# Optimization experiments

Measured on AMD Instinct MI355X. Metric: run time of the kernel, lower is better.

Reference implementation:

```python
import jax, jax.numpy as jnp
import numpy as np

B, V, NQ, D, HEADS, FF, NL = 2, 8, 336, 256, 8, 1024, 6
H_IMG, W_IMG = 512, 512


def setup_inputs() -> dict:
    key = jax.random.key(0)
    ks = iter(jax.random.split(key, 48))
    def n(shape, s=0.02):
        return jax.random.normal(next(ks), shape, dtype=jnp.float32) * s
    inp = {}
    inp["tgt"] = jnp.zeros((B, NQ, D), jnp.float32)
    inp["query_pos"] = jax.random.normal(next(ks), (B, NQ, D), jnp.float32)
    inp["reference_points"] = jax.random.uniform(next(ks), (B, NQ, 3), dtype=jnp.float32)
    inp["feat0"] = jax.random.normal(next(ks), (B, V, D, 64, 64), jnp.float32)
    inp["feat1"] = jax.random.normal(next(ks), (B, V, D, 32, 32), jnp.float32)
    inp["feat2"] = jax.random.normal(next(ks), (B, V, D, 16, 16), jnp.float32)
    # cameras: near-identity rotations, translation pushed +2 in z so points project in front
    inp["camera_R"] = jnp.broadcast_to(jnp.eye(3, dtype=jnp.float32), (B, V, 3, 3)) + n((B, V, 3, 3), 0.1)
    T = n((B, V, 3), 0.1)
    inp["camera_T"] = T.at[..., 2].add(2.0)
    K = jnp.array([[500.0, 0.0, 256.0], [0.0, 500.0, 256.0], [0.0, 0.0, 1.0]], jnp.float32)
    inp["camera_K"] = jnp.broadcast_to(K, (B, V, 3, 3))
    # decoder params (stacked over NL layers)
    inp["Wqkv"] = n((NL, 3 * D, D)); inp["bqkv"] = jnp.zeros((NL, 3 * D), jnp.float32)
    inp["Wo"] = n((NL, D, D));       inp["bo"] = jnp.zeros((NL, D), jnp.float32)
    inp["ln1_g"] = jnp.ones((NL, D), jnp.float32); inp["ln1_b"] = jnp.zeros((NL, D), jnp.float32)
    inp["Wproj"] = n((NL, D, D));    inp["bproj"] = jnp.zeros((NL, D), jnp.float32)
    inp["pn_g"] = jnp.ones((NL, D), jnp.float32); inp["pn_b"] = jnp.zeros((NL, D), jnp.float32)
    inp["W1"] = n((NL, FF, D));      inp["b1"] = jnp.zeros((NL, FF), jnp.float32)
    inp["W2"] = n((NL, D, FF));      inp["b2"] = jnp.zeros((NL, D), jnp.float32)
    inp["ln2_g"] = jnp.ones((NL, D), jnp.float32); inp["ln2_b"] = jnp.zeros((NL, D), jnp.float32)
    inp["pose_W0"] = n((D, D)); inp["pose_b0"] = jnp.zeros((D,), jnp.float32)
    inp["pose_W1"] = n((D, D)); inp["pose_b1"] = jnp.zeros((D,), jnp.float32)
    inp["pose_W2"] = n((3, D)); inp["pose_b2"] = jnp.zeros((3,), jnp.float32)
    inp["cls_W"] = n((1, D));   inp["cls_b"] = jnp.zeros((1,), jnp.float32)
    return inp


def _layer_norm(x, g, b):
    m = x.mean(-1, keepdims=True)
    v = ((x - m) ** 2).mean(-1, keepdims=True)
    return (x - m) * jax.lax.rsqrt(v + 1e-5) * g + b


def _project(pts, R, T, K):
    # pts (B,NQ,3) -> cam coords per view: pts @ R^T + T
    p = jnp.einsum('bqc,bvdc->bvqd', pts, R) + T[:, :, None, :]  # (B,V,NQ,3)
    z = jnp.clip(p[..., 2], 0.1, None)
    fx = K[..., 0, 0][:, :, None]; fy = K[..., 1, 1][:, :, None]
    cx = K[..., 0, 2][:, :, None]; cy = K[..., 1, 2][:, :, None]
    u = p[..., 0] * fx / z + cx
    v = p[..., 1] * fy / z + cy
    un = 2.0 * u / (W_IMG - 1) - 1.0
    vn = 2.0 * v / (H_IMG - 1) - 1.0
    mask = (un > -1.0) & (un < 1.0) & (vn > -1.0) & (vn < 1.0) & (p[..., 2] > 0)
    return jnp.stack([un, vn], -1), mask  # (B,V,NQ,2), (B,V,NQ)


def _sample(feats, grid):
    # bilinear point sampling == F.grid_sample(align_corners=False, padding_mode='zeros')
    C, Hh, Ww = feats.shape[2], feats.shape[3], feats.shape[4]
    f = feats.reshape(B * V, C, Hh, Ww)
    g = grid.reshape(B * V, NQ, 2)
    x = (g[..., 0] + 1.0) * Ww * 0.5 - 0.5
    y = (g[..., 1] + 1.0) * Hh * 0.5 - 0.5
    x0f = jnp.floor(x); y0f = jnp.floor(y)
    ix0 = x0f.astype(jnp.int32); iy0 = y0f.astype(jnp.int32)
    ix1 = ix0 + 1; iy1 = iy0 + 1
    wx1 = (x - x0f)[:, None, :]; wx0 = 1.0 - wx1
    wy1 = (y - y0f)[:, None, :]; wy0 = 1.0 - wy1
    def gat(ix, iy):
        valid = ((ix >= 0) & (ix < Ww) & (iy >= 0) & (iy < Hh)).astype(f.dtype)[:, None, :]
        ixc = jnp.clip(ix, 0, Ww - 1); iyc = jnp.clip(iy, 0, Hh - 1)
        vals = jax.vmap(lambda ff, yy, xx: ff[:, yy, xx])(f, iyc, ixc)  # (BV,C,NQ)
        return vals * valid
    out = (gat(ix0, iy0) * wy0 * wx0 + gat(ix1, iy0) * wy0 * wx1 +
           gat(ix0, iy1) * wy1 * wx0 + gat(ix1, iy1) * wy1 * wx1)
    return out.reshape(B, V, C, NQ).transpose(0, 1, 3, 2)  # (B,V,NQ,C)


def _mha(xq, xv, Wqkv, bqkv, Wo, bo):
    hd = D // HEADS
    q = (xq @ Wqkv[:D].T + bqkv[:D]).reshape(B, NQ, HEADS, hd)
    k = (xq @ Wqkv[D:2 * D].T + bqkv[D:2 * D]).reshape(B, NQ, HEADS, hd)
    v = (xv @ Wqkv[2 * D:].T + bqkv[2 * D:]).reshape(B, NQ, HEADS, hd)
    att = jax.nn.softmax(jnp.einsum('bqhd,bkhd->bhqk', q, k) * (1.0 / np.sqrt(hd)), axis=-1)
    o = jnp.einsum('bhqk,bkhd->bqhd', att, v).reshape(B, NQ, D)
    return o @ Wo.T + bo


def reference(tgt, query_pos, reference_points, feat0, feat1, feat2, camera_R, camera_T, camera_K,
              Wqkv, bqkv, Wo, bo, ln1_g, ln1_b, Wproj, bproj, pn_g, pn_b,
              W1, b1, W2, b2, ln2_g, ln2_b,
              pose_W0, pose_b0, pose_W1, pose_b1, pose_W2, pose_b2, cls_W, cls_b):
    out = tgt
    ref = reference_points
    feats = (feat0, feat1, feat2)
    logits_all, poses_all = [], []
    for l in range(NL):
        # self-attention (dropout = eval identity)
        qk = out + query_pos
        out = _layer_norm(out + _mha(qk, out, Wqkv[l], bqkv[l], Wo[l], bo[l]), ln1_g[l], ln1_b[l])
        # projective attention: project 3D refs, grid-sample all levels, mask-fuse across views
        grid, mask = _project(ref, camera_R, camera_T, camera_K)
        ms = (_sample(feats[0], grid) + _sample(feats[1], grid) + _sample(feats[2], grid)) / 3.0
        vm = mask[..., None].astype(out.dtype)  # (B,V,NQ,1)
        fused = (ms * vm).sum(1) / jnp.clip(vm.sum(1), 1.0, None)  # (B,NQ,D)
        out = _layer_norm(out + fused @ Wproj[l].T + bproj[l], pn_g[l], pn_b[l])
        # FFN
        ffn = jax.nn.relu(out @ W1[l].T + b1[l]) @ W2[l].T + b2[l]
        out = _layer_norm(out + ffn, ln2_g[l], ln2_b[l])
        # iterative pose refinement + classification head
        h = jax.nn.relu(out @ pose_W0.T + pose_b0)
        h = jax.nn.relu(h @ pose_W1.T + pose_b1)
        ref = ref + h @ pose_W2.T + pose_b2
        logits_all.append(out @ cls_W.T + cls_b)
        poses_all.append(ref)
    # (NL,B,NQ,1) logits ++ (NL,B,NQ,3) poses -> (NL,B,NQ,4)
    return jnp.concatenate([jnp.stack(logits_all), jnp.stack(poses_all)], axis=-1)
```

## Files before the change

### kernel.cpp

```cpp
#include <hip/hip_runtime.h>
#include <math.h>

#define BB 2
#define VV 8
#define NQ 336
#define DD 256
#define HEADS 8
#define HD 32
#define FF 1024
#define NL 6
#define BQ (BB*NQ)
#define W_IMG 512
#define H_IMG 512
#define MROWS BQ

__device__ __forceinline__ void job_transpose3(float* tile, int b,
                                               const float* __restrict__ f0,
                                               const float* __restrict__ f1,
                                               const float* __restrict__ f2,
                                               float* __restrict__ o0,
                                               float* __restrict__ o1,
                                               float* __restrict__ o2) {
    const float* src; float* dst; int HW, ptiles;
    if (b < 4096)      { src = f0; dst = o0; HW = 4096; ptiles = 128; }
    else if (b < 5120) { b -= 4096; src = f1; dst = o1; HW = 1024; ptiles = 32; }
    else               { b -= 5120; src = f2; dst = o2; HW = 256;  ptiles = 8;  }
    int cg = b & 1;
    int pt = (b >> 1) % ptiles;
    int bv = (b >> 1) / ptiles;
    int d0 = cg * 128, p0 = pt * 32;
    int t = threadIdx.x;
    int chb = t >> 3, px4 = (t & 7) * 4;
    #pragma unroll
    for (int pass = 0; pass < 4; ++pass) {
        int ch = pass * 32 + chb;
        float4 v = *(const float4*)(src + ((size_t)(bv * DD + d0 + ch)) * HW + p0 + px4);
        tile[ch * 33 + px4 + 0] = v.x; tile[ch * 33 + px4 + 1] = v.y;
        tile[ch * 33 + px4 + 2] = v.z; tile[ch * 33 + px4 + 3] = v.w;
    }
    __syncthreads();
    int c4 = (t & 31) * 4, pxb = t >> 5;
    #pragma unroll
    for (int pass = 0; pass < 4; ++pass) {
        int px = pass * 8 + pxb;
        float4 o;
        o.x = tile[(c4 + 0) * 33 + px];
        o.y = tile[(c4 + 1) * 33 + px];
        o.z = tile[(c4 + 2) * 33 + px];
        o.w = tile[(c4 + 3) * 33 + px];
        *(float4*)(dst + ((size_t)bv * HW + p0 + px) * DD + d0 + c4) = o;
    }
}

__global__ __launch_bounds__(256) void init_k(const float* __restrict__ tgt,
                                              const float* __restrict__ qp,
                                              const float* __restrict__ refpts,
                                              float* __restrict__ x,
                                              float* __restrict__ xq,
                                              float* __restrict__ refb) {
    int i = blockIdx.x * 256 + threadIdx.x;
    float4 tv = ((const float4*)tgt)[i];
    float4 qv = ((const float4*)qp)[i];
    ((float4*)x)[i] = tv;
    ((float4*)xq)[i] = make_float4(tv.x + qv.x, tv.y + qv.y, tv.z + qv.z, tv.w + qv.w);
    if (i < BQ * 3) refb[i] = refpts[i];
}

__device__ __forceinline__ void job_qkv(float* sm, int bid,
                                        const float* __restrict__ Aq,
                                        const float* __restrict__ Ax,
                                        const float* __restrict__ W,
                                        const float* __restrict__ bias,
                                        float* __restrict__ Qp,
                                        float* __restrict__ Kp,
                                        float* __restrict__ Vp) {
    float* At = sm;
    float* Wt = sm + 1088;
    int t = threadIdx.x;
    int m0 = (bid % 21) * 32;
    int ncol = bid / 21;
    int n0 = ncol * 64;
    const float* A = (ncol < 8) ? Aq : Ax;
    int tx = t & 15, ty = t >> 4;
    int nc = n0 + tx * 4;
    float acc0[4], acc1[4];
    {
        float4 bv = *(const float4*)(bias + nc);
        acc0[0] = bv.x; acc0[1] = bv.y; acc0[2] = bv.z; acc0[3] = bv.w;
        acc1[0] = bv.x; acc1[1] = bv.y; acc1[2] = bv.z; acc1[3] = bv.w;
    }
    int am = t >> 3, ak4 = (t & 7) * 4;
    for (int kt = 0; kt < 8; ++kt) {
        int kk = kt * 32;
        __syncthreads();
        {
            float4 v = *(const float4*)(A + (size_t)(m0 + am) * DD + kk + ak4);
            At[(ak4 + 0) * 34 + am] = v.x; At[(ak4 + 1) * 34 + am] = v.y;
            At[(ak4 + 2) * 34 + am] = v.z; At[(ak4 + 3) * 34 + am] = v.w;
        }
        #pragma unroll
        for (int s = 0; s < 2; ++s) {
            int idx = t + s * 256;
            int wn = idx >> 3, wk4 = (idx & 7) * 4;
            float4 v = *(const float4*)(W + (size_t)(n0 + wn) * DD + kk + wk4);
            Wt[(wk4 + 0) * 68 + wn] = v.x; Wt[(wk4 + 1) * 68 + wn] = v.y;
            Wt[(wk4 + 2) * 68 + wn] = v.z; Wt[(wk4 + 3) * 68 + wn] = v.w;
        }
        __syncthreads();
        #pragma unroll
        for (int k = 0; k < 32; ++k) {
            float2 av = *(const float2*)&At[k * 34 + ty * 2];
            float4 wv = *(const float4*)&Wt[k * 68 + tx * 4];
            acc0[0] = fmaf(av.x, wv.x, acc0[0]); acc0[1] = fmaf(av.x, wv.y, acc0[1]);
            acc0[2] = fmaf(av.x, wv.z, acc0[2]); acc0[3] = fmaf(av.x, wv.w, acc0[3]);
            acc1[0] = fmaf(av.y, wv.x, acc1[0]); acc1[1] = fmaf(av.y, wv.y, acc1[1]);
            acc1[2] = fmaf(av.y, wv.z, acc1[2]); acc1[3] = fmaf(av.y, wv.w, acc1[3]);
        }
    }
    int mr = m0 + ty * 2;
    int kind = nc >> 8;
    float* base = kind == 0 ? Qp : (kind == 1 ? Kp : Vp);
    int h = (nc >> 5) & 7, d4 = nc & 31;
    #pragma unroll
    for (int i = 0; i < 2; ++i) {
        int m = mr + i;
        int b = m / NQ, q = m - b * NQ;
        float* p = base + ((size_t)((b << 3) + h) * NQ + q) * HD + d4;
        float* src = i == 0 ? acc0 : acc1;
        *(float4*)p = make_float4(src[0], src[1], src[2], src[3]);
    }
}

__device__ __forceinline__ void job_pose(float* sm, int job,
                                         const float* __restrict__ x,
                                         const float* __restrict__ W0, const float* __restrict__ b0,
                                         const float* __restrict__ W1p, const float* __restrict__ b1p,
                                         const float* __restrict__ W2p, const float* __restrict__ b2p,
                                         const float* __restrict__ cW, const float* __restrict__ cb,
                                         float* __restrict__ refb, float* __restrict__ outp) {
    float* sX  = sm;
    float* sH  = sm + 1024;
    float* red = sm + 2048;
    int r0 = job * 4;
    int tid = threadIdx.x;
    ((float4*)sX)[tid] = ((const float4*)(x + (size_t)r0 * DD))[tid];
    __syncthreads();
    {
        float a0 = b0[tid], a1 = a0, a2 = a0, a3 = a0;
        const float* wp = W0 + (size_t)tid * DD;
        for (int k = 0; k < DD; k += 4) {
            float4 w  = *(const float4*)(wp + k);
            float4 x0 = *(const float4*)(sX + 0 * DD + k);
            float4 x1 = *(const float4*)(sX + 1 * DD + k);
            float4 x2 = *(const float4*)(sX + 2 * DD + k);
            float4 x3 = *(const float4*)(sX + 3 * DD + k);
            a0 = fmaf(x0.x, w.x, a0); a0 = fmaf(x0.y, w.y, a0); a0 = fmaf(x0.z, w.z, a0); a0 = fmaf(x0.w, w.w, a0);
            a1 = fmaf(x1.x, w.x, a1); a1 = fmaf(x1.y, w.y, a1); a1 = fmaf(x1.z, w.z, a1); a1 = fmaf(x1.w, w.w, a1);
            a2 = fmaf(x2.x, w.x, a2); a2 = fmaf(x2.y, w.y, a2); a2 = fmaf(x2.z, w.z, a2); a2 = fmaf(x2.w, w.w, a2);
            a3 = fmaf(x3.x, w.x, a3); a3 = fmaf(x3.y, w.y, a3); a3 = fmaf(x3.z, w.z, a3); a3 = fmaf(x3.w, w.w, a3);
        }
        sH[0 * DD + tid] = fmaxf(a0, 0.f);
        sH[1 * DD + tid] = fmaxf(a1, 0.f);
        sH[2 * DD + tid] = fmaxf(a2, 0.f);
        sH[3 * DD + tid] = fmaxf(a3, 0.f);
    }
    __syncthreads();
    float h[4];
    {
        float a0 = b1p[tid], a1 = a0, a2 = a0, a3 = a0;
        const float* wp = W1p + (size_t)tid * DD;
        for (int k = 0; k < DD; k += 4) {
            float4 w  = *(const float4*)(wp + k);
            float4 x0 = *(const float4*)(sH + 0 * DD + k);
            float4 x1 = *(const float4*)(sH + 1 * DD + k);
            float4 x2 = *(const float4*)(sH + 2 * DD + k);
            float4 x3 = *(const float4*)(sH + 3 * DD + k);
            a0 = fmaf(x0.x, w.x, a0); a0 = fmaf(x0.y, w.y, a0); a0 = fmaf(x0.z, w.z, a0); a0 = fmaf(x0.w, w.w, a0);
            a1 = fmaf(x1.x, w.x, a1); a1 = fmaf(x1.y, w.y, a1); a1 = fmaf(x1.z, w.z, a1); a1 = fmaf(x1.w, w.w, a1);
            a2 = fmaf(x2.x, w.x, a2); a2 = fmaf(x2.y, w.y, a2); a2 = fmaf(x2.z, w.z, a2); a2 = fmaf(x2.w, w.w, a2);
            a3 = fmaf(x3.x, w.x, a3); a3 = fmaf(x3.y, w.y, a3); a3 = fmaf(x3.z, w.z, a3); a3 = fmaf(x3.w, w.w, a3);
        }
        h[0] = fmaxf(a0, 0.f); h[1] = fmaxf(a1, 0.f); h[2] = fmaxf(a2, 0.f); h[3] = fmaxf(a3, 0.f);
    }
    float w2a = W2p[tid], w2b = W2p[DD + tid], w2c = W2p[2 * DD + tid], cw = cW[tid];
    float v[4][4];
    #pragma unroll
    for (int r = 0; r < 4; ++r) {
        v[r][0] = h[r] * w2a;
        v[r][1] = h[r] * w2b;
        v[r][2] = h[r] * w2c;
        v[r][3] = sX[r * DD + tid] * cw;
    }
    #pragma unroll
    for (int o2 = 32; o2 > 0; o2 >>= 1) {
        #pragma unroll
        for (int r = 0; r < 4; ++r) {
            #pragma unroll
            for (int c = 0; c < 4; ++c) v[r][c] += __shfl_xor(v[r][c], o2);
        }
    }
    int wid = tid >> 6, lane = tid & 63;
    if (lane == 0) {
        #pragma unroll
        for (int r = 0; r < 4; ++r) {
            #pragma unroll
            for (int c = 0; c < 4; ++c) red[(r * 4 + c) * 4 + wid] = v[r][c];
        }
    }
    __syncthreads();
    if (tid < 4) {
        int r = tid;
        float d0 = red[(r * 4 + 0) * 4 + 0] + red[(r * 4 + 0) * 4 + 1] + red[(r * 4 + 0) * 4 + 2] + red[(r * 4 + 0) * 4 + 3] + b2p[0];
        float d1 = red[(r * 4 + 1) * 4 + 0] + red[(r * 4 + 1) * 4 + 1] + red[(r * 4 + 1) * 4 + 2] + red[(r * 4 + 1) * 4 + 3] + b2p[1];
        float d2 = red[(r * 4 + 2) * 4 + 0] + red[(r * 4 + 2) * 4 + 1] + red[(r * 4 + 2) * 4 + 2] + red[(r * 4 + 2) * 4 + 3] + b2p[2];
        float cl = red[(r * 4 + 3) * 4 + 0] + red[(r * 4 + 3) * 4 + 1] + red[(r * 4 + 3) * 4 + 2] + red[(r * 4 + 3) * 4 + 3] + cb[0];
        int row = r0 + r;
        float rx = refb[(size_t)row * 3 + 0] + d0;
        float ry = refb[(size_t)row * 3 + 1] + d1;
        float rz = refb[(size_t)row * 3 + 2] + d2;
        refb[(size_t)row * 3 + 0] = rx;
        refb[(size_t)row * 3 + 1] = ry;
        refb[(size_t)row * 3 + 2] = rz;
        outp[(size_t)row * 4 + 0] = cl;
        outp[(size_t)row * 4 + 1] = rx;
        outp[(size_t)row * 4 + 2] = ry;
        outp[(size_t)row * 4 + 3] = rz;
    }
}

__global__ __launch_bounds__(256) void qkv_pose(const float* __restrict__ xq,
                                                const float* __restrict__ x,
                                                const float* __restrict__ Wqkv,
                                                const float* __restrict__ bqkv,
                                                float* __restrict__ Qp,
                                                float* __restrict__ Kp,
                                                float* __restrict__ Vp,
                                                const float* __restrict__ pW0, const float* __restrict__ pb0,
                                                const float* __restrict__ pW1, const float* __restrict__ pb1,
                                                const float* __restrict__ pW2, const float* __restrict__ pb2,
                                                const float* __restrict__ cW, const float* __restrict__ cb,
                                                float* __restrict__ refb, float* __restrict__ outp) {
    __shared__ float sm[3264];
    if (blockIdx.x < 252)
        job_qkv(sm, blockIdx.x, xq, x, Wqkv, bqkv, Qp, Kp, Vp);
    else
        job_pose(sm, blockIdx.x - 252, x, pW0, pb0, pW1, pb1, pW2, pb2, cW, cb, refb, outp);
}

__global__ __launch_bounds__(256) void qkv_tr(const float* __restrict__ xq,
                                              const float* __restrict__ x,
                                              const float* __restrict__ Wqkv,
                                              const float* __restrict__ bqkv,
                                              float* __restrict__ Qp,
                                              float* __restrict__ Kp,
                                              float* __restrict__ Vp,
                                              const float* __restrict__ f0,
                                              const float* __restrict__ f1,
                                              const float* __restrict__ f2,
                                              float* __restrict__ o0,
                                              float* __restrict__ o1,
                                              float* __restrict__ o2) {
    __shared__ float sm[4224];
    if (blockIdx.x < 252)
        job_qkv(sm, blockIdx.x, xq, x, Wqkv, bqkv, Qp, Kp, Vp);
    else
        job_transpose3(sm, blockIdx.x - 252, f0, f1, f2, o0, o1, o2);
}

__global__ __launch_bounds__(256) void pose_only(const float* __restrict__ x,
                                                 const float* __restrict__ pW0, const float* __restrict__ pb0,
                                                 const float* __restrict__ pW1, const float* __restrict__ pb1,
                                                 const float* __restrict__ pW2, const float* __restrict__ pb2,
                                                 const float* __restrict__ cW, const float* __restrict__ cb,
                                                 float* __restrict__ refb, float* __restrict__ outp) {
    __shared__ float sm[2112];
    job_pose(sm, blockIdx.x, x, pW0, pb0, pW1, pb1, pW2, pb2, cW, cb, refb, outp);
}

__global__ __launch_bounds__(256) void attn_fused(const float* __restrict__ Qp,
                                                  const float* __restrict__ Kp,
                                                  const float* __restrict__ Vp,
                                                  float* __restrict__ O) {
    __shared__ float sm[15264];
    float* S   = sm;
    float* KT  = sm + 11008;
    float* U   = sm + 13184;
    float* inv = sm + 15232;
    int blk = blockIdx.x;
    int bh = blk & 15, qt = blk >> 4;
    int t = threadIdx.x;
    const float scale = 0.17677669529663687f;
    const float* Qb = Qp + (size_t)bh * NQ * HD;
    const float* Kb = Kp + (size_t)bh * NQ * HD;
    const float* Vb = Vp + (size_t)bh * NQ * HD;
    {
        int ql = t >> 3, d4 = (t & 7) * 4;
        int qg = qt * 32 + ql;
        float4 v = (qg < NQ) ? *(const float4*)(Qb + (size_t)qg * HD + d4)
                             : make_float4(0.f, 0.f, 0.f, 0.f);
        U[(d4 + 0) * 36 + ql] = v.x * scale;
        U[(d4 + 1) * 36 + ql] = v.y * scale;
        U[(d4 + 2) * 36 + ql] = v.z * scale;
        U[(d4 + 3) * 36 + ql] = v.w * scale;
    }
    int tx = t & 15, ty = t >> 4;
    for (int kt = 0; kt < 6; ++kt) {
        __syncthreads();
        #pragma unroll
        for (int s = 0; s < 2; ++s) {
            int idx = t + s * 256;
            int kl = idx >> 3, d4 = (idx & 7) * 4;
            int kg = kt * 64 + kl;
            float4 v = (kg < NQ) ? *(const float4*)(Kb + (size_t)kg * HD + d4)
                                 : make_float4(0.f, 0.f, 0.f, 0.f);
            KT[(d4 + 0) * 68 + kl] = v.x; KT[(d4 + 1) * 68 + kl] = v.y;
            KT[(d4 + 2) * 68 + kl] = v.z; KT[(d4 + 3) * 68 + kl] = v.w;
        }
        __syncthreads();
        float a0[4] = {0, 0, 0, 0}, a1[4] = {0, 0, 0, 0};
        #pragma unroll
        for (int k = 0; k < 32; ++k) {
            float2 qv = *(const float2*)&U[k * 36 + ty * 2];
            float4 kv = *(const float4*)&KT[k * 68 + tx * 4];
            a0[0] = fmaf(qv.x, kv.x, a0[0]); a0[1] = fmaf(qv.x, kv.y, a0[1]);
            a0[2] = fmaf(qv.x, kv.z, a0[2]); a0[3] = fmaf(qv.x, kv.w, a0[3]);
            a1[0] = fmaf(qv.y, kv.x, a1[0]); a1[1] = fmaf(qv.y, kv.y, a1[1]);
            a1[2] = fmaf(qv.y, kv.z, a1[2]); a1[3] = fmaf(qv.y, kv.w, a1[3]);
        }
        int col = kt * 64 + tx * 4;
        if (col < NQ) {
            *(float4*)&S[(ty * 2 + 0) * 344 + col] = make_float4(a0[0], a0[1], a0[2], a0[3]);
            *(float4*)&S[(ty * 2 + 1) * 344 + col] = make_float4(a1[0], a1[1], a1[2], a1[3]);
        }
    }
    __syncthreads();
    {
        int r = t >> 3, cg = t & 7;
        float* row = S + (size_t)r * 344;
        float m = -1e30f;
        for (int i = 0; i < 42; ++i) m = fmaxf(m, row[cg + 8 * i]);
        m = fmaxf(m, __shfl_xor(m, 1));
        m = fmaxf(m, __shfl_xor(m, 2));
        m = fmaxf(m, __shfl_xor(m, 4));
        float ssum = 0.f;
        for (int i = 0; i < 42; ++i) {
            float e = expf(row[cg + 8 * i] - m);
            row[cg + 8 * i] = e;
            ssum += e;
        }
        ssum += __shfl_xor(ssum, 1);
        ssum += __shfl_xor(ssum, 2);
        ssum += __shfl_xor(ssum, 4);
        if (cg == 0) inv[r] = 1.f / ssum;
    }
    int q = t >> 3, d0 = (t & 7) * 4;
    float acc[4] = {0, 0, 0, 0};
    for (int kt = 0; kt < 6; ++kt) {
        __syncthreads();
        #pragma unroll
        for (int s = 0; s < 2; ++s) {
            int idx = t + s * 256;
            int kl = idx >> 3, d4 = (idx & 7) * 4;
            int kg = kt * 64 + kl;
            float4 v = (kg < NQ) ? *(const float4*)(Vb + (size_t)kg * HD + d4)
                                 : make_float4(0.f, 0.f, 0.f, 0.f);
            *(float4*)&U[kl * 32 + d4] = v;
        }
        __syncthreads();
        int kmax = (kt == 5) ? 16 : 64;
        const float* Srow = S + (size_t)q * 344 + kt * 64;
        #pragma unroll 8
        for (int kk = 0; kk < kmax; ++kk) {
            float p = Srow[kk];
            float4 vv = *(const float4*)&U[kk * 32 + d0];
            acc[0] = fmaf(p, vv.x, acc[0]); acc[1] = fmaf(p, vv.y, acc[1]);
            acc[2] = fmaf(p, vv.z, acc[2]); acc[3] = fmaf(p, vv.w, acc[3]);
        }
    }
    float iv = inv[q];
    int qg = qt * 32 + q;
    int b = bh >> 3, h = bh & 7;
    if (qg < NQ)
        *(float4*)(O + ((size_t)(b * NQ + qg)) * DD + h * HD + d0) =
            make_float4(acc[0] * iv, acc[1] * iv, acc[2] * iv, acc[3] * iv);
}

__device__ __forceinline__ void job_gemm_ln(float* sm, int r0,
                                            const float* __restrict__ A,
                                            const float* __restrict__ Wt,
                                            const float* __restrict__ bias,
                                            const float* __restrict__ gam,
                                            const float* __restrict__ bet,
                                            float* __restrict__ x) {
    float* sA    = sm;
    float* redS  = sm + 1024;
    float* redS2 = sm + 1040;
    float* mu    = sm + 1056;
    float* ri    = sm + 1060;
    int j = threadIdx.x;
    ((float4*)sA)[j] = ((const float4*)(A + (size_t)r0 * DD))[j];
    __syncthreads();
    float acc0 = bias[j], acc1 = acc0, acc2 = acc0, acc3 = acc0;
    const float* wp = Wt + (size_t)j * DD;
    for (int k = 0; k < DD; k += 4) {
        float4 w  = *(const float4*)(wp + k);
        float4 a0 = *(const float4*)(sA + 0 * DD + k);
        float4 a1 = *(const float4*)(sA + 1 * DD + k);
        float4 a2 = *(const float4*)(sA + 2 * DD + k);
        float4 a3 = *(const float4*)(sA + 3 * DD + k);
        acc0 = fmaf(a0.x, w.x, acc0); acc0 = fmaf(a0.y, w.y, acc0); acc0 = fmaf(a0.z, w.z, acc0); acc0 = fmaf(a0.w, w.w, acc0);
        acc1 = fmaf(a1.x, w.x, acc1); acc1 = fmaf(a1.y, w.y, acc1); acc1 = fmaf(a1.z, w.z, acc1); acc1 = fmaf(a1.w, w.w, acc1);
        acc2 = fmaf(a2.x, w.x, acc2); acc2 = fmaf(a2.y, w.y, acc2); acc2 = fmaf(a2.z, w.z, acc2); acc2 = fmaf(a2.w, w.w, acc2);
        acc3 = fmaf(a3.x, w.x, acc3); acc3 = fmaf(a3.y, w.y, acc3); acc3 = fmaf(a3.z, w.z, acc3); acc3 = fmaf(a3.w, w.w, acc3);
    }
    float val[4];
    val[0] = x[(size_t)(r0 + 0) * DD + j] + acc0;
    val[1] = x[(size_t)(r0 + 1) * DD + j] + acc1;
    val[2] = x[(size_t)(r0 + 2) * DD + j] + acc2;
    val[3] = x[(size_t)(r0 + 3) * DD + j] + acc3;
    float s[4], s2[4];
    #pragma unroll
    for (int r = 0; r < 4; ++r) { s[r] = val[r]; s2[r] = val[r] * val[r]; }
    #pragma unroll
    for (int o2 = 32; o2 > 0; o2 >>= 1) {
        #pragma unroll
        for (int r = 0; r < 4; ++r) {
            s[r]  += __shfl_xor(s[r],  o2);
            s2[r] += __shfl_xor(s2[r], o2);
        }
    }
    int wid = j >> 6, lane = j & 63;
    if (lane == 0) {
        #pragma unroll
        for (int r = 0; r < 4; ++r) { redS[r * 4 + wid] = s[r]; redS2[r * 4 + wid] = s2[r]; }
    }
    __syncthreads();
    if (j < 4) {
        int r = j;
        float ts  = redS[r * 4 + 0]  + redS[r * 4 + 1]  + redS[r * 4 + 2]  + redS[r * 4 + 3];
        float ts2 = redS2[r * 4 + 0] + redS2[r * 4 + 1] + redS2[r * 4 + 2] + redS2[r * 4 + 3];
        float mean = ts * (1.f / DD);
        float var = ts2 * (1.f / DD) - mean * mean;
        mu[r] = mean;
        ri[r] = rsqrtf(var + 1e-5f);
    }
    __syncthreads();
    float g = gam[j], be = bet[j];
    #pragma unroll
    for (int r = 0; r < 4; ++r)
        x[(size_t)(r0 + r) * DD + j] = (val[r] - mu[r]) * ri[r] * g + be;
}

template <bool TRANSPOSED>
__device__ __forceinline__ void job_sample(float* sm, int row,
                                           const float* __restrict__ f0,
                                           const float* __restrict__ f1,
                                           const float* __restrict__ f2,
                                           const float* __restrict__ refb,
                                           const float* __restrict__ Rm,
                                           const float* __restrict__ Tm,
                                           const float* __restrict__ Km,
                                           float* __restrict__ fused) {
    float* sg    = sm;
    float* sPart = sm + 32;
    int t = threadIdx.x;
    int b = row / NQ;
    if (t < 8) {
        int bv = b * VV + t;
        const float* r = refb + (size_t)row * 3;
        const float* R = Rm + (size_t)bv * 9;
        const float* T = Tm + (size_t)bv * 3;
        const float* K = Km + (size_t)bv * 9;
        float p0 = R[0] * r[0] + R[1] * r[1] + R[2] * r[2] + T[0];
        float p1 = R[3] * r[0] + R[4] * r[1] + R[5] * r[2] + T[1];
        float p2 = R[6] * r[0] + R[7] * r[1] + R[8] * r[2] + T[2];
        float z = fmaxf(p2, 0.1f);
        float u  = p0 * K[0] / z + K[2];
        float vv = p1 * K[4] / z + K[5];
        float un = 2.f * u  / (float)(W_IMG - 1) - 1.f;
        float vn = 2.f * vv / (float)(H_IMG - 1) - 1.f;
        bool m = (un > -1.f) && (un < 1.f) && (vn > -1.f) && (vn < 1.f) && (p2 > 0.f);
        sg[t * 3 + 0] = un; sg[t * 3 + 1] = vn; sg[t * 3 + 2] = m ? 1.f : 0.f;
    }
    __syncthreads();
    int v = t >> 5, cg = t & 31;
    int ch0 = cg * 8;
    float acc[8] = {0, 0, 0, 0, 0, 0, 0, 0};
    float m = sg[v * 3 + 2];
    if (m != 0.f) {
        float un = sg[v * 3 + 0], vn = sg[v * 3 + 1];
        int bv = b * VV + v;
        const float* fl[3] = { f0, f1, f2 };
        const int Hs[3] = { 64, 32, 16 };
        #pragma unroll
        for (int lev = 0; lev < 3; ++lev) {
            int Hh = Hs[lev], Ww = Hs[lev];
            const float* f = fl[lev];
            float xx = (un + 1.f) * Ww * 0.5f - 0.5f;
            float yy = (vn + 1.f) * Hh * 0.5f - 0.5f;
            float x0f = floorf(xx), y0f = floorf(yy);
            int ix0 = (int)x0f, iy0 = (int)y0f;
            float wx1 = xx - x0f, wx0 = 1.f - wx1;
            float wy1 = yy - y0f, wy0 = 1.f - wy1;
            #pragma unroll
            for (int tap = 0; tap < 4; ++tap) {
                int ix = ix0 + (tap & 1);
                int iy = iy0 + (tap >> 1);
                float wgt = ((tap & 1) ? wx1 : wx0) * ((tap >> 1) ? wy1 : wy0);
                if (ix >= 0 && ix < Ww && iy >= 0 && iy < Hh) {
                    if (TRANSPOSED) {
                        const float* p = f + ((size_t)bv * Hh * Ww + (size_t)iy * Ww + ix) * DD + ch0;
                        float4 va = *(const float4*)p;
                        float4 vb = *(const float4*)(p + 4);
                        acc[0] = fmaf(wgt, va.x, acc[0]); acc[1] = fmaf(wgt, va.y, acc[1]);
                        acc[2] = fmaf(wgt, va.z, acc[2]); acc[3] = fmaf(wgt, va.w, acc[3]);
                        acc[4] = fmaf(wgt, vb.x, acc[4]); acc[5] = fmaf(wgt, vb.y, acc[5]);
                        acc[6] = fmaf(wgt, vb.z, acc[6]); acc[7] = fmaf(wgt, vb.w, acc[7]);
                    } else {
                        #pragma unroll
                        for (int c = 0; c < 8; ++c) {
                            float vv2 = f[(((size_t)bv * DD + ch0 + c) * Hh + iy) * Ww + ix];
                            acc[c] = fmaf(wgt, vv2, acc[c]);
                        }
                    }
                }
            }
        }
    }
    #pragma unroll
    for (int c = 0; c < 8; ++c) sPart[v * 258 + ch0 + c] = acc[c] * (1.f / 3.f);
    __syncthreads();
    float cnt = sg[2] + sg[5] + sg[8] + sg[11] + sg[14] + sg[17] + sg[20] + sg[23];
    float s = 0.f;
    #pragma unroll
    for (int v2 = 0; v2 < 8; ++v2) s += sPart[v2 * 258 + t];
    fused[(size_t)row * DD + t] = s / fmaxf(cnt, 1.f);
}

template <bool TRANSPOSED>
__global__ __launch_bounds__(256) void oproj_sample(const float* __restrict__ attn_o,
                                                    const float* __restrict__ Wo,
                                                    const float* __restrict__ bo,
                                                    const float* __restrict__ gam,
                                                    const float* __restrict__ bet,
                                                    float* __restrict__ x,
                                                    const float* __restrict__ f0,
                                                    const float* __restrict__ f1,
                                                    const float* __restrict__ f2,
                                                    const float* __restrict__ refb,
                                                    const float* __restrict__ Rm,
                                                    const float* __restrict__ Tm,
                                                    const float* __restrict__ Km,
                                                    float* __restrict__ fused) {
    __shared__ float sm[2112];
    if (blockIdx.x < 168)
        job_gemm_ln(sm, blockIdx.x * 4, attn_o, Wo, bo, gam, bet, x);
    else
        job_sample<TRANSPOSED>(sm, blockIdx.x - 168, f0, f1, f2, refb, Rm, Tm, Km, fused);
}

__global__ __launch_bounds__(256) void gemm4_res_ln(const float* __restrict__ A,
                                                    const float* __restrict__ Wt,
                                                    const float* __restrict__ bias,
                                                    const float* __restrict__ gam,
                                                    const float* __restrict__ bet,
                                                    float* __restrict__ x) {
    __shared__ float sm[1064];
    job_gemm_ln(sm, blockIdx.x * 4, A, Wt, bias, gam, bet, x);
}

template <int MODE>
__global__ __launch_bounds__(256) void gemm_tile(const float* __restrict__ A,
                                                 const float* __restrict__ W,
                                                 const float* __restrict__ bias,
                                                 float* __restrict__ C,
                                                 int Ktot, int Kper, int Nout) {
    __shared__ float At[32][34];
    __shared__ float Wt[32][68];
    int t = threadIdx.x;
    int m0 = blockIdx.x * 32;
    int n0 = blockIdx.y * 64;
    int kz = blockIdx.z;
    int kofs = kz * Kper;
    int tx = t & 15, ty = t >> 4;
    int nc = n0 + tx * 4;
    float acc0[4], acc1[4];
    {
        float4 bv = make_float4(0.f, 0.f, 0.f, 0.f);
        if (bias && kz == 0) bv = *(const float4*)(bias + nc);
        acc0[0] = bv.x; acc0[1] = bv.y; acc0[2] = bv.z; acc0[3] = bv.w;
        acc1[0] = bv.x; acc1[1] = bv.y; acc1[2] = bv.z; acc1[3] = bv.w;
    }
    int am = t >> 3, ak4 = (t & 7) * 4;
    int ktiles = Kper >> 5;
    for (int kt = 0; kt < ktiles; ++kt) {
        int kk = kofs + kt * 32;
        __syncthreads();
        {
            float4 v = *(const float4*)(A + (size_t)(m0 + am) * Ktot + kk + ak4);
            At[ak4 + 0][am] = v.x; At[ak4 + 1][am] = v.y;
            At[ak4 + 2][am] = v.z; At[ak4 + 3][am] = v.w;
        }
        #pragma unroll
        for (int s = 0; s < 2; ++s) {
            int idx = t + s * 256;
            int wn = idx >> 3, wk4 = (idx & 7) * 4;
            float4 v = *(const float4*)(W + (size_t)(n0 + wn) * Ktot + kk + wk4);
            Wt[wk4 + 0][wn] = v.x; Wt[wk4 + 1][wn] = v.y;
            Wt[wk4 + 2][wn] = v.z; Wt[wk4 + 3][wn] = v.w;
        }
        __syncthreads();
        #pragma unroll
        for (int k = 0; k < 32; ++k) {
            float2 av = *(const float2*)&At[k][ty * 2];
            float4 wv = *(const float4*)&Wt[k][tx * 4];
            acc0[0] = fmaf(av.x, wv.x, acc0[0]); acc0[1] = fmaf(av.x, wv.y, acc0[1]);
            acc0[2] = fmaf(av.x, wv.z, acc0[2]); acc0[3] = fmaf(av.x, wv.w, acc0[3]);
            acc1[0] = fmaf(av.y, wv.x, acc1[0]); acc1[1] = fmaf(av.y, wv.y, acc1[1]);
            acc1[2] = fmaf(av.y, wv.z, acc1[2]); acc1[3] = fmaf(av.y, wv.w, acc1[3]);
        }
    }
    if (MODE == 1) {
        #pragma unroll
        for (int j = 0; j < 4; ++j) { acc0[j] = fmaxf(acc0[j], 0.f); acc1[j] = fmaxf(acc1[j], 0.f); }
    }
    int mr = m0 + ty * 2;
    float* Cb = C + (size_t)kz * MROWS * Nout;
    *(float4*)(Cb + (size_t)mr * Nout + nc)       = make_float4(acc0[0], acc0[1], acc0[2], acc0[3]);
    *(float4*)(Cb + (size_t)(mr + 1) * Nout + nc) = make_float4(acc1[0], acc1[1], acc1[2], acc1[3]);
}

template <int NP>
__global__ __launch_bounds__(256) void ln_res(float* __restrict__ x,
                                              const float* __restrict__ C,
                                              const float* __restrict__ gam,
                                              const float* __restrict__ bet,
                                              const float* __restrict__ qp,
                                              float* __restrict__ xq) {
    __shared__ float redS[4][4], redS2[4][4];
    __shared__ float mu[4], ri[4];
    int r0 = blockIdx.x * 4;
    int j = threadIdx.x;
    float val[4];
    #pragma unroll
    for (int r = 0; r < 4; ++r) {
        float a = x[(size_t)(r0 + r) * DD + j];
        #pragma unroll
        for (int p = 0; p < NP; ++p) a += C[(size_t)p * MROWS * DD + (size_t)(r0 + r) * DD + j];
        val[r] = a;
    }
    float s[4], s2[4];
    #pragma unroll
    for (int r = 0; r < 4; ++r) { s[r] = val[r]; s2[r] = val[r] * val[r]; }
    #pragma unroll
    for (int o = 32; o > 0; o >>= 1) {
        #pragma unroll
        for (int r = 0; r < 4; ++r) {
            s[r]  += __shfl_xor(s[r],  o);
            s2[r] += __shfl_xor(s2[r], o);
        }
    }
    int wid = j >> 6, lane = j & 63;
    if (lane == 0) {
        #pragma unroll
        for (int r = 0; r < 4; ++r) { redS[r][wid] = s[r]; redS2[r][wid] = s2[r]; }
    }
    __syncthreads();
    if (j < 4) {
        int r = j;
        float ts  = redS[r][0]  + redS[r][1]  + redS[r][2]  + redS[r][3];
        float ts2 = redS2[r][0] + redS2[r][1] + redS2[r][2] + redS2[r][3];
        float mean = ts * (1.f / DD);
        float var = ts2 * (1.f / DD) - mean * mean;
        mu[r] = mean;
        ri[r] = rsqrtf(var + 1e-5f);
    }
    __syncthreads();
    float g = gam[j], be = bet[j];
    #pragma unroll
    for (int r = 0; r < 4; ++r) {
        float o = (val[r] - mu[r]) * ri[r] * g + be;
        x[(size_t)(r0 + r) * DD + j] = o;
        if (qp) xq[(size_t)(r0 + r) * DD + j] = o + qp[(size_t)(r0 + r) * DD + j];
    }
}

extern "C" void kernel_launch(void* const* d_in, const int* in_sizes, int n_in,
                              void* d_out, int out_size, void* d_ws, size_t ws_size,
                              hipStream_t stream) {
    const float* tgt       = (const float*)d_in[0];
    const float* query_pos = (const float*)d_in[1];
    const float* refpts    = (const float*)d_in[2];
    const float* feat0     = (const float*)d_in[3];
    const float* feat1     = (const float*)d_in[4];
    const float* feat2     = (const float*)d_in[5];
    const float* camR      = (const float*)d_in[6];
    const float* camT      = (const float*)d_in[7];
    const float* camK      = (const float*)d_in[8];
    const float* Wqkv      = (const float*)d_in[9];
    const float* bqkv      = (const float*)d_in[10];
    const float* Wo        = (const float*)d_in[11];
    const float* bo        = (const float*)d_in[12];
    const float* ln1_g     = (const float*)d_in[13];
    const float* ln1_b     = (const float*)d_in[14];
    const float* Wproj     = (const float*)d_in[15];
    const float* bproj     = (const float*)d_in[16];
    const float* pn_g      = (const float*)d_in[17];
    const float* pn_b      = (const float*)d_in[18];
    const float* W1        = (const float*)d_in[19];
    const float* b1        = (const float*)d_in[20];
    const float* W2        = (const float*)d_in[21];
    const float* b2        = (const float*)d_in[22];
    const float* ln2_g     = (const float*)d_in[23];
    const float* ln2_b     = (const float*)d_in[24];
    const float* pose_W0   = (const float*)d_in[25];
    const float* pose_b0   = (const float*)d_in[26];
    const float* pose_W1   = (const float*)d_in[27];
    const float* pose_b1   = (const float*)d_in[28];
    const float* pose_W2   = (const float*)d_in[29];
    const float* pose_b2   = (const float*)d_in[30];
    const float* cls_W     = (const float*)d_in[31];
    const float* cls_b     = (const float*)d_in[32];
    float* out = (float*)d_out;

    float* w = (float*)d_ws;
    size_t off = 0;
    auto alloc = [&](size_t n) { float* p = w + off; off += n; return p; };
    float* x      = alloc((size_t)BQ * DD);
    float* xq     = alloc((size_t)BQ * DD);
    float* Qp     = alloc((size_t)BB * HEADS * NQ * HD);
    float* Kp     = alloc((size_t)BB * HEADS * NQ * HD);
    float* Vp     = alloc((size_t)BB * HEADS * NQ * HD);
    float* attn_o = alloc((size_t)BQ * DD);
    float* fused  = alloc((size_t)BQ * DD);
    float* ffh    = alloc((size_t)BQ * FF);
    float* ctmp   = alloc((size_t)4 * BQ * DD);
    float* refb   = alloc((size_t)BQ * 3 + 64);
    size_t base_floats = off;
    size_t featT_floats = (size_t)BB * VV * DD * (64 * 64 + 32 * 32 + 16 * 16);
    bool useT = ws_size >= (base_floats + featT_floats) * sizeof(float);
    float *fT0 = nullptr, *fT1 = nullptr, *fT2 = nullptr;
    if (useT) {
        fT0 = alloc((size_t)BB * VV * 64 * 64 * DD);
        fT1 = alloc((size_t)BB * VV * 32 * 32 * DD);
        fT2 = alloc((size_t)BB * VV * 16 * 16 * DD);
    }

    init_k<<<168, 256, 0, stream>>>(tgt, query_pos, refpts, x, xq, refb);

    for (int l = 0; l < NL; ++l) {
        if (l == 0 && useT) {
            qkv_tr<<<252 + 5376, 256, 0, stream>>>(
                xq, x, Wqkv, bqkv, Qp, Kp, Vp,
                feat0, feat1, feat2, fT0, fT1, fT2);
        } else {
            qkv_pose<<<252 + (l > 0 ? 168 : 0), 256, 0, stream>>>(
                xq, x, Wqkv + (size_t)l * 3 * DD * DD, bqkv + (size_t)l * 3 * DD, Qp, Kp, Vp,
                pose_W0, pose_b0, pose_W1, pose_b1, pose_W2, pose_b2, cls_W, cls_b,
                refb, out + (size_t)(l - 1) * BQ * 4);
        }
        attn_fused<<<176, 256, 0, stream>>>(Qp, Kp, Vp, attn_o);
        if (useT)
            oproj_sample<true><<<840, 256, 0, stream>>>(
                attn_o, Wo + (size_t)l * DD * DD, bo + (size_t)l * DD,
                ln1_g + (size_t)l * DD, ln1_b + (size_t)l * DD, x,
                fT0, fT1, fT2, refb, camR, camT, camK, fused);
        else
            oproj_sample<false><<<840, 256, 0, stream>>>(
                attn_o, Wo + (size_t)l * DD * DD, bo + (size_t)l * DD,
                ln1_g + (size_t)l * DD, ln1_b + (size_t)l * DD, x,
                feat0, feat1, feat2, refb, camR, camT, camK, fused);
        gemm4_res_ln<<<BQ / 4, 256, 0, stream>>>(
            fused, Wproj + (size_t)l * DD * DD, bproj + (size_t)l * DD,
            pn_g + (size_t)l * DD, pn_b + (size_t)l * DD, x);
        gemm_tile<1><<<dim3(21, 16, 1), 256, 0, stream>>>(
            x, W1 + (size_t)l * FF * DD, b1 + (size_t)l * FF, ffh, DD, DD, FF);
        gemm_tile<0><<<dim3(21, 4, 4), 256, 0, stream>>>(
            ffh, W2 + (size_t)l * DD * FF, b2 + (size_t)l * DD, ctmp, FF, FF / 4, DD);
        ln_res<4><<<BQ / 4, 256, 0, stream>>>(
            x, ctmp, ln2_g + (size_t)l * DD, ln2_b + (size_t)l * DD, query_pos, xq);
    }
    pose_only<<<BQ / 4, 256, 0, stream>>>(
        x, pose_W0, pose_b0, pose_W1, pose_b1, pose_W2, pose_b2, cls_W, cls_b,
        refb, out + (size_t)(NL - 1) * BQ * 4);
}
```

Baseline: 842.7 us.

## Fuse attention with grid sampling and merge both output projections with layernorms

Attention now runs as 16-query-tile blocks inside the same launch as the multi-view grid-sampling blocks, which removes one launch per layer and lets the two independent stages overlap. The attention output projection with its layernorm and the fused-feature projection with its layernorm are merged into one kernel that handles two rows per block, keeping the intermediate row in shared memory. This works because sampling depends only on the reference points, not on the attention result. The cost is larger shared memory in the combined kernel, which may lower occupancy for the sampling blocks, and the two-rows-per-block GEMM rereads the weights more often.

```diff
diff --git a/kernel.cpp b/kernel.cpp
--- a/kernel.cpp
+++ b/kernel.cpp
@@ -277,33 +277,32 @@
     job_pose(sm, blockIdx.x, x, pW0, pb0, pW1, pb1, pW2, pb2, cW, cb, refb, outp);
 }
 
-__global__ __launch_bounds__(256) void attn_fused(const float* __restrict__ Qp,
-                                                  const float* __restrict__ Kp,
-                                                  const float* __restrict__ Vp,
-                                                  float* __restrict__ O) {
-    __shared__ float sm[15264];
+__device__ __forceinline__ void job_attn16(float* sm, int blk,
+                                           const float* __restrict__ Qp,
+                                           const float* __restrict__ Kp,
+                                           const float* __restrict__ Vp,
+                                           float* __restrict__ O) {
     float* S   = sm;
-    float* KT  = sm + 11008;
-    float* U   = sm + 13184;
-    float* inv = sm + 15232;
-    int blk = blockIdx.x;
+    float* KT  = sm + 5504;
+    float* U   = sm + 7680;
+    float* inv = sm + 9728;
     int bh = blk & 15, qt = blk >> 4;
     int t = threadIdx.x;
     const float scale = 0.17677669529663687f;
     const float* Qb = Qp + (size_t)bh * NQ * HD;
     const float* Kb = Kp + (size_t)bh * NQ * HD;
     const float* Vb = Vp + (size_t)bh * NQ * HD;
-    {
+    if (t < 128) {
         int ql = t >> 3, d4 = (t & 7) * 4;
-        int qg = qt * 32 + ql;
+        int qg = qt * 16 + ql;
         float4 v = (qg < NQ) ? *(const float4*)(Qb + (size_t)qg * HD + d4)
                              : make_float4(0.f, 0.f, 0.f, 0.f);
-        U[(d4 + 0) * 36 + ql] = v.x * scale;
-        U[(d4 + 1) * 36 + ql] = v.y * scale;
-        U[(d4 + 2) * 36 + ql] = v.z * scale;
-        U[(d4 + 3) * 36 + ql] = v.w * scale;
-    }
-    int tx = t & 15, ty = t >> 4;
+        U[(d4 + 0) * 20 + ql] = v.x * scale;
+        U[(d4 + 1) * 20 + ql] = v.y * scale;
+        U[(d4 + 2) * 20 + ql] = v.z * scale;
+        U[(d4 + 3) * 20 + ql] = v.w * scale;
+    }
+    int r = t >> 4, tx = t & 15;
     for (int kt = 0; kt < 6; ++kt) {
         __syncthreads();
         #pragma unroll
@@ -317,44 +316,41 @@
             KT[(d4 + 2) * 68 + kl] = v.z; KT[(d4 + 3) * 68 + kl] = v.w;
         }
         __syncthreads();
-        float a0[4] = {0, 0, 0, 0}, a1[4] = {0, 0, 0, 0};
+        float a0 = 0.f, a1 = 0.f, a2 = 0.f, a3 = 0.f;
         #pragma unroll
         for (int k = 0; k < 32; ++k) {
-            float2 qv = *(const float2*)&U[k * 36 + ty * 2];
+            float qv = U[k * 20 + r];
             float4 kv = *(const float4*)&KT[k * 68 + tx * 4];
-            a0[0] = fmaf(qv.x, kv.x, a0[0]); a0[1] = fmaf(qv.x, kv.y, a0[1]);
-            a0[2] = fmaf(qv.x, kv.z, a0[2]); a0[3] = fmaf(qv.x, kv.w, a0[3]);
-            a1[0] = fmaf(qv.y, kv.x, a1[0]); a1[1] = fmaf(qv.y, kv.y, a1[1]);
-            a1[2] = fmaf(qv.y, kv.z, a1[2]); a1[3] = fmaf(qv.y, kv.w, a1[3]);
+            a0 = fmaf(qv, kv.x, a0); a1 = fmaf(qv, kv.y, a1);
+            a2 = fmaf(qv, kv.z, a2); a3 = fmaf(qv, kv.w, a3);
         }
         int col = kt * 64 + tx * 4;
-        if (col < NQ) {
-            *(float4*)&S[(ty * 2 + 0) * 344 + col] = make_float4(a0[0], a0[1], a0[2], a0[3]);
-            *(float4*)&S[(ty * 2 + 1) * 344 + col] = make_float4(a1[0], a1[1], a1[2], a1[3]);
-        }
+        if (col < NQ)
+            *(float4*)&S[r * 344 + col] = make_float4(a0, a1, a2, a3);
     }
     __syncthreads();
     {
-        int r = t >> 3, cg = t & 7;
         float* row = S + (size_t)r * 344;
         float m = -1e30f;
-        for (int i = 0; i < 42; ++i) m = fmaxf(m, row[cg + 8 * i]);
+        for (int i = 0; i < 21; ++i) m = fmaxf(m, row[tx + 16 * i]);
         m = fmaxf(m, __shfl_xor(m, 1));
         m = fmaxf(m, __shfl_xor(m, 2));
         m = fmaxf(m, __shfl_xor(m, 4));
+        m = fmaxf(m, __shfl_xor(m, 8));
         float ssum = 0.f;
-        for (int i = 0; i < 42; ++i) {
-            float e = expf(row[cg + 8 * i] - m);
-            row[cg + 8 * i] = e;
+        for (int i = 0; i < 21; ++i) {
+            float e = expf(row[tx + 16 * i] - m);
+            row[tx + 16 * i] = e;
             ssum += e;
         }
         ssum += __shfl_xor(ssum, 1);
         ssum += __shfl_xor(ssum, 2);
         ssum += __shfl_xor(ssum, 4);
-        if (cg == 0) inv[r] = 1.f / ssum;
-    }
-    int q = t >> 3, d0 = (t & 7) * 4;
-    float acc[4] = {0, 0, 0, 0};
+        ssum += __shfl_xor(ssum, 8);
+        if (tx == 0) inv[r] = 1.f / ssum;
+    }
+    int d0 = tx * 2;
+    float acc0 = 0.f, acc1 = 0.f;
     for (int kt = 0; kt < 6; ++kt) {
         __syncthreads();
         #pragma unroll
@@ -368,87 +364,20 @@
         }
         __syncthreads();
         int kmax = (kt == 5) ? 16 : 64;
-        const float* Srow = S + (size_t)q * 344 + kt * 64;
+        const float* Srow = S + (size_t)r * 344 + kt * 64;
         #pragma unroll 8
         for (int kk = 0; kk < kmax; ++kk) {
             float p = Srow[kk];
-            float4 vv = *(const float4*)&U[kk * 32 + d0];
-            acc[0] = fmaf(p, vv.x, acc[0]); acc[1] = fmaf(p, vv.y, acc[1]);
-            acc[2] = fmaf(p, vv.z, acc[2]); acc[3] = fmaf(p, vv.w, acc[3]);
-        }
-    }
-    float iv = inv[q];
-    int qg = qt * 32 + q;
+            float2 vv = *(const float2*)&U[kk * 32 + d0];
+            acc0 = fmaf(p, vv.x, acc0); acc1 = fmaf(p, vv.y, acc1);
+        }
+    }
+    float iv = inv[r];
+    int qg = qt * 16 + r;
     int b = bh >> 3, h = bh & 7;
     if (qg < NQ)
-        *(float4*)(O + ((size_t)(b * NQ + qg)) * DD + h * HD + d0) =
-            make_float4(acc[0] * iv, acc[1] * iv, acc[2] * iv, acc[3] * iv);
-}
-
-__device__ __forceinline__ void job_gemm_ln(float* sm, int r0,
-                                            const float* __restrict__ A,
-                                            const float* __restrict__ Wt,
-                                            const float* __restrict__ bias,
-                                            const float* __restrict__ gam,
-                                            const float* __restrict__ bet,
-                                            float* __restrict__ x) {
-    float* sA    = sm;
-    float* redS  = sm + 1024;
-    float* redS2 = sm + 1040;
-    float* mu    = sm + 1056;
-    float* ri    = sm + 1060;
-    int j = threadIdx.x;
-    ((float4*)sA)[j] = ((const float4*)(A + (size_t)r0 * DD))[j];
-    __syncthreads();
-    float acc0 = bias[j], acc1 = acc0, acc2 = acc0, acc3 = acc0;
-    const float* wp = Wt + (size_t)j * DD;
-    for (int k = 0; k < DD; k += 4) {
-        float4 w  = *(const float4*)(wp + k);
-        float4 a0 = *(const float4*)(sA + 0 * DD + k);
-        float4 a1 = *(const float4*)(sA + 1 * DD + k);
-        float4 a2 = *(const float4*)(sA + 2 * DD + k);
-        float4 a3 = *(const float4*)(sA + 3 * DD + k);
-        acc0 = fmaf(a0.x, w.x, acc0); acc0 = fmaf(a0.y, w.y, acc0); acc0 = fmaf(a0.z, w.z, acc0); acc0 = fmaf(a0.w, w.w, acc0);
-        acc1 = fmaf(a1.x, w.x, acc1); acc1 = fmaf(a1.y, w.y, acc1); acc1 = fmaf(a1.z, w.z, acc1); acc1 = fmaf(a1.w, w.w, acc1);
-        acc2 = fmaf(a2.x, w.x, acc2); acc2 = fmaf(a2.y, w.y, acc2); acc2 = fmaf(a2.z, w.z, acc2); acc2 = fmaf(a2.w, w.w, acc2);
-        acc3 = fmaf(a3.x, w.x, acc3); acc3 = fmaf(a3.y, w.y, acc3); acc3 = fmaf(a3.z, w.z, acc3); acc3 = fmaf(a3.w, w.w, acc3);
-    }
-    float val[4];
-    val[0] = x[(size_t)(r0 + 0) * DD + j] + acc0;
-    val[1] = x[(size_t)(r0 + 1) * DD + j] + acc1;
-    val[2] = x[(size_t)(r0 + 2) * DD + j] + acc2;
-    val[3] = x[(size_t)(r0 + 3) * DD + j] + acc3;
-    float s[4], s2[4];
-    #pragma unroll
-    for (int r = 0; r < 4; ++r) { s[r] = val[r]; s2[r] = val[r] * val[r]; }
-    #pragma unroll
-    for (int o2 = 32; o2 > 0; o2 >>= 1) {
-        #pragma unroll
-        for (int r = 0; r < 4; ++r) {
-            s[r]  += __shfl_xor(s[r],  o2);
-            s2[r] += __shfl_xor(s2[r], o2);
-        }
-    }
-    int wid = j >> 6, lane = j & 63;
-    if (lane == 0) {
-        #pragma unroll
-        for (int r = 0; r < 4; ++r) { redS[r * 4 + wid] = s[r]; redS2[r * 4 + wid] = s2[r]; }
-    }
-    __syncthreads();
-    if (j < 4) {
-        int r = j;
-        float ts  = redS[r * 4 + 0]  + redS[r * 4 + 1]  + redS[r * 4 + 2]  + redS[r * 4 + 3];
-        float ts2 = redS2[r * 4 + 0] + redS2[r * 4 + 1] + redS2[r * 4 + 2] + redS2[r * 4 + 3];
-        float mean = ts * (1.f / DD);
-        float var = ts2 * (1.f / DD) - mean * mean;
-        mu[r] = mean;
-        ri[r] = rsqrtf(var + 1e-5f);
-    }
-    __syncthreads();
-    float g = gam[j], be = bet[j];
-    #pragma unroll
-    for (int r = 0; r < 4; ++r)
-        x[(size_t)(r0 + r) * DD + j] = (val[r] - mu[r]) * ri[r] * g + be;
+        *(float2*)(O + ((size_t)(b * NQ + qg)) * DD + h * HD + d0) =
+            make_float2(acc0 * iv, acc1 * iv);
 }
 
 template <bool TRANSPOSED>
@@ -538,35 +467,116 @@
 }
 
 template <bool TRANSPOSED>
-__global__ __launch_bounds__(256) void oproj_sample(const float* __restrict__ attn_o,
+__global__ __launch_bounds__(256) void attn_sample(const float* __restrict__ Qp,
+                                                   const float* __restrict__ Kp,
+                                                   const float* __restrict__ Vp,
+                                                   float* __restrict__ O,
+                                                   const float* __restrict__ f0,
+                                                   const float* __restrict__ f1,
+                                                   const float* __restrict__ f2,
+                                                   const float* __restrict__ refb,
+                                                   const float* __restrict__ Rm,
+                                                   const float* __restrict__ Tm,
+                                                   const float* __restrict__ Km,
+                                                   float* __restrict__ fused) {
+    __shared__ float sm[9744];
+    if (blockIdx.x < 672)
+        job_sample<TRANSPOSED>(sm, blockIdx.x, f0, f1, f2, refb, Rm, Tm, Km, fused);
+    else
+        job_attn16(sm, blockIdx.x - 672, Qp, Kp, Vp, O);
+}
+
+__global__ __launch_bounds__(256) void dual_gemm_ln(const float* __restrict__ attn_o,
                                                     const float* __restrict__ Wo,
                                                     const float* __restrict__ bo,
-                                                    const float* __restrict__ gam,
-                                                    const float* __restrict__ bet,
-                                                    float* __restrict__ x,
-                                                    const float* __restrict__ f0,
-                                                    const float* __restrict__ f1,
-                                                    const float* __restrict__ f2,
-                                                    const float* __restrict__ refb,
-                                                    const float* __restrict__ Rm,
-                                                    const float* __restrict__ Tm,
-                                                    const float* __restrict__ Km,
-                                                    float* __restrict__ fused) {
-    __shared__ float sm[2112];
-    if (blockIdx.x < 168)
-        job_gemm_ln(sm, blockIdx.x * 4, attn_o, Wo, bo, gam, bet, x);
-    else
-        job_sample<TRANSPOSED>(sm, blockIdx.x - 168, f0, f1, f2, refb, Rm, Tm, Km, fused);
-}
-
-__global__ __launch_bounds__(256) void gemm4_res_ln(const float* __restrict__ A,
-                                                    const float* __restrict__ Wt,
-                                                    const float* __restrict__ bias,
-                                                    const float* __restrict__ gam,
-                                                    const float* __restrict__ bet,
+                                                    const float* __restrict__ g1,
+                                                    const float* __restrict__ be1,
+                                                    const float* __restrict__ fusedIn,
+                                                    const float* __restrict__ Wp,
+                                                    const float* __restrict__ bp,
+                                                    const float* __restrict__ g2,
+                                                    const float* __restrict__ be2,
                                                     float* __restrict__ x) {
-    __shared__ float sm[1064];
-    job_gemm_ln(sm, blockIdx.x * 4, A, Wt, bias, gam, bet, x);
+    __shared__ float sA[2 * DD];
+    __shared__ float sX1[2 * DD];
+    __shared__ float redS[8], redS2[8], mu[2], ri[2];
+    int r0 = blockIdx.x * 2;
+    int j = threadIdx.x;
+    ((float2*)sA)[j] = ((const float2*)(attn_o + (size_t)r0 * DD))[j];
+    __syncthreads();
+    {
+        float acc0 = bo[j], acc1 = acc0;
+        const float* wp = Wo + (size_t)j * DD;
+        for (int k = 0; k < DD; k += 4) {
+            float4 w  = *(const float4*)(wp + k);
+            float4 a0 = *(const float4*)(sA + k);
+            float4 a1 = *(const float4*)(sA + DD + k);
+            acc0 = fmaf(a0.x, w.x, acc0); acc0 = fmaf(a0.y, w.y, acc0);
+            acc0 = fmaf(a0.z, w.z, acc0); acc0 = fmaf(a0.w, w.w, acc0);
+            acc1 = fmaf(a1.x, w.x, acc1); acc1 = fmaf(a1.y, w.y, acc1);
+            acc1 = fmaf(a1.z, w.z, acc1); acc1 = fmaf(a1.w, w.w, acc1);
+        }
+        float val0 = x[(size_t)r0 * DD + j] + acc0;
+        float val1 = x[(size_t)(r0 + 1) * DD + j] + acc1;
+        float s0 = val0, q0 = val0 * val0, s1 = val1, q1 = val1 * val1;
+        #pragma unroll
+        for (int o2 = 32; o2 > 0; o2 >>= 1) {
+            s0 += __shfl_xor(s0, o2); q0 += __shfl_xor(q0, o2);
+            s1 += __shfl_xor(s1, o2); q1 += __shfl_xor(q1, o2);
+        }
+        int wid = j >> 6, lane = j & 63;
+        if (lane == 0) { redS[wid] = s0; redS2[wid] = q0; redS[4 + wid] = s1; redS2[4 + wid] = q1; }
+        __syncthreads();
+        if (j < 2) {
+            float ts  = redS[j * 4 + 0] + redS[j * 4 + 1] + redS[j * 4 + 2] + redS[j * 4 + 3];
+            float ts2 = redS2[j * 4 + 0] + redS2[j * 4 + 1] + redS2[j * 4 + 2] + redS2[j * 4 + 3];
+            float mean = ts * (1.f / DD);
+            float var = ts2 * (1.f / DD) - mean * mean;
+            mu[j] = mean; ri[j] = rsqrtf(var + 1e-5f);
+        }
+        __syncthreads();
+        float g = g1[j], be = be1[j];
+        sX1[j]      = (val0 - mu[0]) * ri[0] * g + be;
+        sX1[DD + j] = (val1 - mu[1]) * ri[1] * g + be;
+    }
+    ((float2*)sA)[j] = ((const float2*)(fusedIn + (size_t)r0 * DD))[j];
+    __syncthreads();
+    {
+        float acc0 = bp[j], acc1 = acc0;
+        const float* wp = Wp + (size_t)j * DD;
+        for (int k = 0; k < DD; k += 4) {
+            float4 w  = *(const float4*)(wp + k);
+            float4 a0 = *(const float4*)(sA + k);
+            float4 a1 = *(const float4*)(sA + DD + k);
+            acc0 = fmaf(a0.x, w.x, acc0); acc0 = fmaf(a0.y, w.y, acc0);
+            acc0 = fmaf(a0.z, w.z, acc0); acc0 = fmaf(a0.w, w.w, acc0);
+            acc1 = fmaf(a1.x, w.x, acc1); acc1 = fmaf(a1.y, w.y, acc1);
+            acc1 = fmaf(a1.z, w.z, acc1); acc1 = fmaf(a1.w, w.w, acc1);
+        }
+        float val0 = sX1[j] + acc0;
+        float val1 = sX1[DD + j] + acc1;
+        float s0 = val0, q0 = val0 * val0, s1 = val1, q1 = val1 * val1;
+        #pragma unroll
+        for (int o2 = 32; o2 > 0; o2 >>= 1) {
+            s0 += __shfl_xor(s0, o2); q0 += __shfl_xor(q0, o2);
+            s1 += __shfl_xor(s1, o2); q1 += __shfl_xor(q1, o2);
+        }
+        int wid = j >> 6, lane = j & 63;
+        __syncthreads();
+        if (lane == 0) { redS[wid] = s0; redS2[wid] = q0; redS[4 + wid] = s1; redS2[4 + wid] = q1; }
+        __syncthreads();
+        if (j < 2) {
+            float ts  = redS[j * 4 + 0] + redS[j * 4 + 1] + redS[j * 4 + 2] + redS[j * 4 + 3];
+            float ts2 = redS2[j * 4 + 0] + redS2[j * 4 + 1] + redS2[j * 4 + 2] + redS2[j * 4 + 3];
+            float mean = ts * (1.f / DD);
+            float var = ts2 * (1.f / DD) - mean * mean;
+            mu[j] = mean; ri[j] = rsqrtf(var + 1e-5f);
+        }
+        __syncthreads();
+        float g = g2[j], be = be2[j];
+        x[(size_t)r0 * DD + j]       = (val0 - mu[0]) * ri[0] * g + be;
+        x[(size_t)(r0 + 1) * DD + j] = (val1 - mu[1]) * ri[1] * g + be;
+    }
 }
 
 template <int MODE>
@@ -759,18 +769,15 @@
                 pose_W0, pose_b0, pose_W1, pose_b1, pose_W2, pose_b2, cls_W, cls_b,
                 refb, out + (size_t)(l - 1) * BQ * 4);
         }
-        attn_fused<<<176, 256, 0, stream>>>(Qp, Kp, Vp, attn_o);
         if (useT)
-            oproj_sample<true><<<840, 256, 0, stream>>>(
-                attn_o, Wo + (size_t)l * DD * DD, bo + (size_t)l * DD,
-                ln1_g + (size_t)l * DD, ln1_b + (size_t)l * DD, x,
-                fT0, fT1, fT2, refb, camR, camT, camK, fused);
+            attn_sample<true><<<1024, 256, 0, stream>>>(
+                Qp, Kp, Vp, attn_o, fT0, fT1, fT2, refb, camR, camT, camK, fused);
         else
-            oproj_sample<false><<<840, 256, 0, stream>>>(
-                attn_o, Wo + (size_t)l * DD * DD, bo + (size_t)l * DD,
-                ln1_g + (size_t)l * DD, ln1_b + (size_t)l * DD, x,
-                feat0, feat1, feat2, refb, camR, camT, camK, fused);
-        gemm4_res_ln<<<BQ / 4, 256, 0, stream>>>(
+            attn_sample<false><<<1024, 256, 0, stream>>>(
+                Qp, Kp, Vp, attn_o, feat0, feat1, feat2, refb, camR, camT, camK, fused);
+        dual_gemm_ln<<<336, 256, 0, stream>>>(
+            attn_o, Wo + (size_t)l * DD * DD, bo + (size_t)l * DD,
+            ln1_g + (size_t)l * DD, ln1_b + (size_t)l * DD,
             fused, Wproj + (size_t)l * DD * DD, bproj + (size_t)l * DD,
             pn_g + (size_t)l * DD, pn_b + (size_t)l * DD, x);
         gemm_tile<1><<<dim3(21, 16, 1), 256, 0, stream>>>(
```

Result: slower. 926.8 us (+10.0%).
